# Optimization experiments

Hardware: AMD Instinct MI355X
Metric: run time of the kernel (lower is better)

The kernel has to match this reference:

```python
import jax, jax.numpy as jnp
import numpy as np
import math

D_MODEL = 768
N_HEADS = 12
D_HEAD = D_MODEL // N_HEADS
B, T = 2, 2048
EPS = 1e-5


def _layernorm(x, g, b):
    mu = jnp.mean(x, axis=-1, keepdims=True)
    var = jnp.var(x, axis=-1, keepdims=True)
    return (x - mu) * jax.lax.rsqrt(var + EPS) * g + b


def setup_inputs() -> dict:
    key = jax.random.key(0)
    ks = jax.random.split(key, 16)
    s = 0.02
    inp = {
        "x": jax.random.normal(ks[0], (B, T, D_MODEL), jnp.float32),
        "q_pos": jax.random.normal(ks[1], (B, N_HEADS, T, D_HEAD), jnp.float32),
        "k_pos": jax.random.normal(ks[2], (B, N_HEADS, T, D_HEAD), jnp.float32),
        "causal_mask": jnp.triu(jnp.ones((T, T), dtype=bool), k=1),
        "Wq": jax.random.normal(ks[3], (D_MODEL, D_MODEL), jnp.float32) * s,
        "bq": jnp.zeros((D_MODEL,), jnp.float32),
        "Wk": jax.random.normal(ks[4], (D_MODEL, D_MODEL), jnp.float32) * s,
        "bk": jnp.zeros((D_MODEL,), jnp.float32),
        "Wv": jax.random.normal(ks[5], (D_MODEL, D_MODEL), jnp.float32) * s,
        "bv": jnp.zeros((D_MODEL,), jnp.float32),
        "Wo": jax.random.normal(ks[6], (D_MODEL, D_MODEL), jnp.float32) * s,
        "bo": jnp.zeros((D_MODEL,), jnp.float32),
        "ln1_g": jnp.ones((D_MODEL,), jnp.float32),
        "ln1_b": jnp.zeros((D_MODEL,), jnp.float32),
        "ln2_g": jnp.ones((D_MODEL,), jnp.float32),
        "ln2_b": jnp.zeros((D_MODEL,), jnp.float32),
        "W1": jax.random.normal(ks[7], (D_MODEL, 4 * D_MODEL), jnp.float32) * s,
        "b1": jnp.zeros((4 * D_MODEL,), jnp.float32),
        "W2": jax.random.normal(ks[8], (4 * D_MODEL, D_MODEL), jnp.float32) * s,
        "b2": jnp.zeros((D_MODEL,), jnp.float32),
    }
    return inp


def reference(x, q_pos, k_pos, causal_mask, Wq, bq, Wk, bk, Wv, bv, Wo, bo,
              ln1_g, ln1_b, ln2_g, ln2_b, W1, b1, W2, b2):
    h = _layernorm(x, ln1_g, ln1_b)  # [B,T,D]
    # project and split heads -> [B,H,T,d]
    def heads(y):
        return y.reshape(B, T, N_HEADS, D_HEAD).transpose(0, 2, 1, 3)
    Qc = heads(h @ Wq + bq)
    Kc = heads(h @ Wk + bk)
    V = heads(h @ Wv + bv)
    scale = math.sqrt(D_HEAD)
    A_X = jnp.einsum('bhqd,bhkd->bhqk', Qc, Kc) / scale
    A_P = jnp.einsum('bhqd,bhkd->bhqk', q_pos, k_pos) / scale
    scores = A_X * A_P  # Hadamard combination of content + positional scores
    scores = jnp.where(causal_mask[None, None, :, :], -jnp.inf, scores)
    attn = jax.nn.softmax(scores, axis=-1)
    out = jnp.einsum('bhqk,bhkd->bhqd', attn, V)  # [B,H,T,d]
    out = out.transpose(0, 2, 1, 3).reshape(B, T, D_MODEL)
    out = out @ Wo + bo
    x = x + out
    h2 = _layernorm(x, ln2_g, ln2_b)
    ffn = jax.nn.gelu(h2 @ W1 + b1, approximate=False) @ W2 + b2
    return x + ffn
```

## Files before the change

kernel.cpp:

```cpp
#include <hip/hip_runtime.h>
#include <hip/hip_bf16.h>
#include <math.h>

#define D_MODEL 768
#define N_HEADS 12
#define D_HEAD  64
#define BATCH   2
#define SEQ     2048
#define ROWS    (BATCH*SEQ)
#define D_FFN   (4*D_MODEL)

typedef short bf16x8 __attribute__((ext_vector_type(8)));
typedef float f32x4  __attribute__((ext_vector_type(4)));

__device__ __forceinline__ short f2bf(float f) {
    __hip_bfloat16 h = __float2bfloat16(f);
    return *reinterpret_cast<short*>(&h);
}

template<int CTRL>
__device__ __forceinline__ float dpp_f(float x) {
    int v = __builtin_amdgcn_update_dpp(0, __float_as_int(x), CTRL, 0xF, 0xF, true);
    return __int_as_float(v);
}
__device__ __forceinline__ float dpp_max16(float x) {
    x = fmaxf(x, dpp_f<0xB1>(x));
    x = fmaxf(x, dpp_f<0x4E>(x));
    x = fmaxf(x, dpp_f<0x141>(x));
    x = fmaxf(x, dpp_f<0x140>(x));
    return x;
}
__device__ __forceinline__ float dpp_sum16(float x) {
    x += dpp_f<0xB1>(x);
    x += dpp_f<0x4E>(x);
    x += dpp_f<0x141>(x);
    x += dpp_f<0x140>(x);
    return x;
}

__global__ __launch_bounds__(256)
void prep_kernel(const float* __restrict__ Wq, const float* __restrict__ Wk,
                 const float* __restrict__ Wv, const float* __restrict__ Wo,
                 const float* __restrict__ W1, const float* __restrict__ W2,
                 const float* __restrict__ q_pos, const float* __restrict__ k_pos,
                 short* __restrict__ WTq, short* __restrict__ WTk,
                 short* __restrict__ WTv, short* __restrict__ WTo,
                 short* __restrict__ WT1, short* __restrict__ WT2,
                 short* __restrict__ qp_bf, short* __restrict__ kp_bf) {
    int id = blockIdx.x;
    if (id >= 6912) {
        int cid = id - 6912;
        bool isq = (cid < 1536);
        int c = isq ? cid : cid - 1536;
        const float* src = isq ? q_pos : k_pos;
        short* dst = isq ? qp_bf : kp_bf;
        int i = (c * 256 + threadIdx.x) * 8;
        float4 a = *reinterpret_cast<const float4*>(src + i);
        float4 b = *reinterpret_cast<const float4*>(src + i + 4);
        bf16x8 r;
        r[0]=f2bf(a.x); r[1]=f2bf(a.y); r[2]=f2bf(a.z); r[3]=f2bf(a.w);
        r[4]=f2bf(b.x); r[5]=f2bf(b.y); r[6]=f2bf(b.z); r[7]=f2bf(b.w);
        *reinterpret_cast<bf16x8*>(dst + i) = r;
        return;
    }
    const float* W; short* WT; int K, N, t;
    if (id < 576)        { W = Wq; WT = WTq; K = 768;  N = 768;  t = id; }
    else if (id < 1152)  { W = Wk; WT = WTk; K = 768;  N = 768;  t = id - 576; }
    else if (id < 1728)  { W = Wv; WT = WTv; K = 768;  N = 768;  t = id - 1152; }
    else if (id < 2304)  { W = Wo; WT = WTo; K = 768;  N = 768;  t = id - 1728; }
    else if (id < 4608)  { W = W1; WT = WT1; K = 768;  N = 3072; t = id - 2304; }
    else                 { W = W2; WT = WT2; K = 3072; N = 768;  t = id - 4608; }
    int nb = N >> 5;
    int n0 = (t % nb) * 32, k0 = (t / nb) * 32;
    __shared__ float tile[32][33];
    int tx = threadIdx.x & 31, ty = threadIdx.x >> 5;
    #pragma unroll
    for (int i = 0; i < 4; ++i)
        tile[ty + 8*i][tx] = W[(size_t)(k0 + ty + 8*i) * N + n0 + tx];
    __syncthreads();
    #pragma unroll
    for (int i = 0; i < 4; ++i)
        WT[(size_t)(n0 + ty + 8*i) * K + k0 + tx] = f2bf(tile[tx][ty + 8*i]);
}

__global__ __launch_bounds__(256)
void transpose_v_kernel(const short* __restrict__ Vm, short* __restrict__ Vt) {
    __shared__ short tile[64][72];
    int kt = blockIdx.x;
    int bh = blockIdx.y;
    int b = bh / N_HEADS, h = bh % N_HEADS;
    int tid = threadIdx.x;
    int row = tid >> 2, c16 = (tid & 3) * 16;
    const short* src = Vm + ((size_t)(b * SEQ) + kt * 64 + row) * D_MODEL + h * 64 + c16;
    *reinterpret_cast<bf16x8*>(&tile[row][c16])     = *reinterpret_cast<const bf16x8*>(src);
    *reinterpret_cast<bf16x8*>(&tile[row][c16 + 8]) = *reinterpret_cast<const bf16x8*>(src + 8);
    __syncthreads();
    int d = tid >> 2, k16 = (tid & 3) * 16;
    short o[16];
    #pragma unroll
    for (int j = 0; j < 16; ++j) o[j] = tile[k16 + j][d];
    short* dst = Vt + ((size_t)bh * 64 + d) * SEQ + kt * 64 + k16;
    *reinterpret_cast<bf16x8*>(dst)     = *reinterpret_cast<bf16x8*>(&o[0]);
    *reinterpret_cast<bf16x8*>(dst + 8) = *reinterpret_cast<bf16x8*>(&o[8]);
}

__global__ __launch_bounds__(256)
void ln_kernel(const float* __restrict__ x, const float* __restrict__ g,
               const float* __restrict__ beta, short* __restrict__ out) {
    int row = blockIdx.x;
    const float* xr = x + (size_t)row * D_MODEL;
    int t = threadIdx.x;
    float v0 = xr[t], v1 = xr[t + 256], v2 = xr[t + 512];
    float s  = v0 + v1 + v2;
    float s2 = v0*v0 + v1*v1 + v2*v2;
    __shared__ float rs[4], rs2[4];
    #pragma unroll
    for (int off = 32; off; off >>= 1) {
        s  += __shfl_down(s, off);
        s2 += __shfl_down(s2, off);
    }
    int wv = t >> 6, ln = t & 63;
    if (ln == 0) { rs[wv] = s; rs2[wv] = s2; }
    __syncthreads();
    float S  = rs[0] + rs[1] + rs[2] + rs[3];
    float S2 = rs2[0] + rs2[1] + rs2[2] + rs2[3];
    float mu  = S * (1.0f / D_MODEL);
    float var = S2 * (1.0f / D_MODEL) - mu * mu;
    float inv = rsqrtf(var + 1e-5f);
    short* orow = out + (size_t)row * D_MODEL;
    orow[t]       = f2bf((v0 - mu) * inv * g[t]       + beta[t]);
    orow[t + 256] = f2bf((v1 - mu) * inv * g[t + 256] + beta[t + 256]);
    orow[t + 512] = f2bf((v2 - mu) * inv * g[t + 512] + beta[t + 512]);
}

template<int ACT, bool RES, bool OUTBF>
__device__ __forceinline__
void gemm_body(const short* __restrict__ A, const short* __restrict__ WT,
               const float* __restrict__ bias, const float* __restrict__ res,
               void* __restrict__ Cout, int M, int N, int Kloop, int Kstride) {
    __shared__ short As[2][128 * 32];
    __shared__ short Bs[2][128 * 32];
    const int tid = threadIdx.x;
    const int w = tid >> 6, lane = tid & 63;
    const int lr = lane & 15, lg = lane >> 4;
    const int wm = w >> 1, wn = w & 1;
    const int bm = blockIdx.y * 128, bn = blockIdx.x * 128;

    f32x4 acc[4][4] = {};

    const int srow = w * 32 + (lane >> 2);
    const int scol = (lane & 3) * 8;
    const short* Ag = A  + (size_t)(bm + srow) * Kstride + scol;
    const short* Bg = WT + (size_t)(bn + srow) * Kstride + scol;

    auto stage = [&](int k0, int buf) {
        #pragma unroll
        for (int r = 0; r < 2; ++r) {
            __builtin_amdgcn_global_load_lds(
                (const __attribute__((address_space(1))) void*)(Ag + (size_t)r * 16 * Kstride + k0),
                (__attribute__((address_space(3))) void*)(&As[buf][0] + w * 1024 + r * 512),
                16, 0, 0);
            __builtin_amdgcn_global_load_lds(
                (const __attribute__((address_space(1))) void*)(Bg + (size_t)r * 16 * Kstride + k0),
                (__attribute__((address_space(3))) void*)(&Bs[buf][0] + w * 1024 + r * 512),
                16, 0, 0);
        }
    };

    stage(0, 0);
    __syncthreads();
    int cur = 0;

    for (int k0 = 0; k0 < Kloop; k0 += 32) {
        if (k0 + 32 < Kloop) stage(k0 + 32, cur ^ 1);

        bf16x8 af[4], bfr[4];
        #pragma unroll
        for (int mi = 0; mi < 4; ++mi)
            af[mi] = *reinterpret_cast<const bf16x8*>(&As[cur][0] + (wm*64 + mi*16 + lr) * 32 + lg*8);
        #pragma unroll
        for (int nj = 0; nj < 4; ++nj)
            bfr[nj] = *reinterpret_cast<const bf16x8*>(&Bs[cur][0] + (wn*64 + nj*16 + lr) * 32 + lg*8);
        __builtin_amdgcn_s_setprio(1);
        #pragma unroll
        for (int mi = 0; mi < 4; ++mi)
            #pragma unroll
            for (int nj = 0; nj < 4; ++nj)
                acc[mi][nj] = __builtin_amdgcn_mfma_f32_16x16x32_bf16(af[mi], bfr[nj], acc[mi][nj], 0, 0, 0);
        __builtin_amdgcn_s_setprio(0);

        __syncthreads();
        cur ^= 1;
    }

    float bias_v[4] = {0.f, 0.f, 0.f, 0.f};
    if constexpr (ACT != 2) {
        #pragma unroll
        for (int nj = 0; nj < 4; ++nj) bias_v[nj] = bias[bn + wn*64 + nj*16 + lr];
    }

    #pragma unroll
    for (int mi = 0; mi < 4; ++mi) {
        #pragma unroll
        for (int j = 0; j < 4; ++j) {
            size_t m = bm + wm*64 + mi*16 + lg*4 + j;
            #pragma unroll
            for (int nj = 0; nj < 4; ++nj) {
                size_t n = bn + wn*64 + nj*16 + lr;
                float v = acc[mi][nj][j] + bias_v[nj];
                if (RES) v += res[m * N + n];
                if (ACT == 1) v = 0.5f * v * (1.0f + erff(v * 0.70710678118f));
                if (OUTBF) ((short*)Cout)[m * N + n] = f2bf(v);
                else       ((float*)Cout)[m * N + n] = v;
            }
        }
    }
}

template<int ACT, bool RES, bool OUTBF>
__global__ __launch_bounds__(256)
void gemm_mfma_kernel(const short* __restrict__ A, const short* __restrict__ WT,
                      const float* __restrict__ bias, const float* __restrict__ res,
                      void* __restrict__ Cout, int M, int N, int K) {
    gemm_body<ACT, RES, OUTBF>(A, WT, bias, res, Cout, M, N, K, K);
}

__global__ __launch_bounds__(256)
void gemm_qkv_kernel(const short* __restrict__ A,
                     const short* __restrict__ WTq, const short* __restrict__ WTk,
                     const short* __restrict__ WTv,
                     const float* __restrict__ bq, const float* __restrict__ bk,
                     const float* __restrict__ bv,
                     short* __restrict__ Qm, short* __restrict__ Km, short* __restrict__ Vm) {
    const short* WT; const float* bias; short* C;
    if (blockIdx.z == 0)      { WT = WTq; bias = bq; C = Qm; }
    else if (blockIdx.z == 1) { WT = WTk; bias = bk; C = Km; }
    else                      { WT = WTv; bias = bv; C = Vm; }
    gemm_body<0, false, true>(A, WT, bias, nullptr, C, ROWS, D_MODEL, D_MODEL, D_MODEL);
}

__global__ __launch_bounds__(256)
void gemm_w2_kernel(const short* __restrict__ mid, const short* __restrict__ WT2,
                    float* __restrict__ P0, float* __restrict__ P1) {
    int z = blockIdx.z;
    gemm_body<2, false, false>(mid + z * 1536, WT2 + z * 1536, nullptr, nullptr,
                               z ? P1 : P0, ROWS, D_MODEL, 1536, D_FFN);
}

__global__ __launch_bounds__(256)
void w2_epi_kernel(const float* __restrict__ P0, const float* __restrict__ P1,
                   const float* __restrict__ b2, const float* __restrict__ x2,
                   float* __restrict__ out) {
    size_t i = ((size_t)blockIdx.x * 256 + threadIdx.x) * 4;
    int n = (int)(i % D_MODEL);
    float4 p0 = *reinterpret_cast<const float4*>(P0 + i);
    float4 p1 = *reinterpret_cast<const float4*>(P1 + i);
    float4 xr = *reinterpret_cast<const float4*>(x2 + i);
    float4 bb = *reinterpret_cast<const float4*>(b2 + n);
    float4 o;
    o.x = p0.x + p1.x + xr.x + bb.x;
    o.y = p0.y + p1.y + xr.y + bb.y;
    o.z = p0.z + p1.z + xr.z + bb.z;
    o.w = p0.w + p1.w + xr.w + bb.w;
    *reinterpret_cast<float4*>(out + i) = o;
}

__global__ __launch_bounds__(256)
void attn_mfma_kernel(const short* __restrict__ Q, const short* __restrict__ K,
                      const short* __restrict__ Vt, const short* __restrict__ qp,
                      const short* __restrict__ kp, short* __restrict__ ao) {
    __shared__ short Ks[2][4096];
    __shared__ short kps[2][4096];
    __shared__ short Vts[2][4096];
    __shared__ short Plds[4][16][76];

    int lin = blockIdx.x;
    int wid = (lin & 7) * 96 + (lin >> 3);
    int bh = wid >> 5;
    int qb = 31 - (wid & 31);
    int b = bh / N_HEADS, h = bh % N_HEADS;
    int tid = threadIdx.x, w = tid >> 6, lane = tid & 63;
    int lr = lane & 15, lg = lane >> 4;

    const short* Kh  = K  + (size_t)(b * SEQ) * D_MODEL + h * 64;
    const short* kph = kp + (size_t)bh * SEQ * 64;
    const short* Vth = Vt + (size_t)bh * 64 * SEQ;

    const int s_sub  = lane >> 3;
    const int s_colb = ((lane & 7) ^ s_sub) << 4;

    auto stage = [&](int kt, int buf) {
        #pragma unroll
        for (int j = 0; j < 2; ++j) {
            int row = (w * 2 + j) * 8 + s_sub;
            int ldsoff = (w * 2 + j) * 1024;
            __builtin_amdgcn_global_load_lds(
                (const __attribute__((address_space(1))) void*)
                    ((const char*)(Kh + (size_t)(kt * 64 + row) * D_MODEL) + s_colb),
                (__attribute__((address_space(3))) void*)((char*)&Ks[buf][0] + ldsoff), 16, 0, 0);
            __builtin_amdgcn_global_load_lds(
                (const __attribute__((address_space(1))) void*)
                    ((const char*)(kph + (size_t)(kt * 64 + row) * 64) + s_colb),
                (__attribute__((address_space(3))) void*)((char*)&kps[buf][0] + ldsoff), 16, 0, 0);
            __builtin_amdgcn_global_load_lds(
                (const __attribute__((address_space(1))) void*)
                    ((const char*)(Vth + (size_t)row * SEQ + kt * 64) + s_colb),
                (__attribute__((address_space(3))) void*)((char*)&Vts[buf][0] + ldsoff), 16, 0, 0);
        }
    };
    auto ldr = [&](const short* base, int row, int halfb) -> bf16x8 {
        int off = row * 128 + ((halfb + lg * 16) ^ ((row & 7) << 4));
        return *reinterpret_cast<const bf16x8*>((const char*)base + off);
    };

    int qbase = qb * 64 + w * 16;
    const short* Qrow  = Q  + ((size_t)(b * SEQ) + qbase + lr) * D_MODEL + h * 64;
    const short* qprow = qp + ((size_t)bh * SEQ + qbase + lr) * 64;
    bf16x8 qf0  = *reinterpret_cast<const bf16x8*>(Qrow + lg * 8);
    bf16x8 qf1  = *reinterpret_cast<const bf16x8*>(Qrow + 32 + lg * 8);
    bf16x8 qpf0 = *reinterpret_cast<const bf16x8*>(qprow + lg * 8);
    bf16x8 qpf1 = *reinterpret_cast<const bf16x8*>(qprow + 32 + lg * 8);

    f32x4 o_acc[4] = {};
    float m_run[4], l_run[4];
    #pragma unroll
    for (int r = 0; r < 4; ++r) { m_run[r] = -1e30f; l_run[r] = 0.f; }

    int nkt = qb + 1;
    stage(0, 0);
    __syncthreads();
    int cur = 0;

    for (int kt = 0; kt < nkt; ++kt) {
        if (kt + 1 < nkt) stage(kt + 1, cur ^ 1);

        const short* Kb  = &Ks[cur][0];
        const short* kpb = &kps[cur][0];
        const short* Vb  = &Vts[cur][0];
        f32x4 sx[4] = {}, sp[4] = {};
        __builtin_amdgcn_s_setprio(1);
        #pragma unroll
        for (int sub = 0; sub < 4; ++sub) {
            int row = sub * 16 + lr;
            bf16x8 kf0 = ldr(Kb, row, 0),  kf1 = ldr(Kb, row, 64);
            bf16x8 kq0 = ldr(kpb, row, 0), kq1 = ldr(kpb, row, 64);
            sx[sub] = __builtin_amdgcn_mfma_f32_16x16x32_bf16(qf0,  kf0, sx[sub], 0, 0, 0);
            sx[sub] = __builtin_amdgcn_mfma_f32_16x16x32_bf16(qf1,  kf1, sx[sub], 0, 0, 0);
            sp[sub] = __builtin_amdgcn_mfma_f32_16x16x32_bf16(qpf0, kq0, sp[sub], 0, 0, 0);
            sp[sub] = __builtin_amdgcn_mfma_f32_16x16x32_bf16(qpf1, kq1, sp[sub], 0, 0, 0);
        }
        __builtin_amdgcn_s_setprio(0);

        float sc[4][4];
        float pmax[4];
        bool diag = (kt == qb);
        #pragma unroll
        for (int r = 0; r < 4; ++r) {
            int row = qbase + lg * 4 + r;
            float mx = -1e30f;
            #pragma unroll
            for (int sub = 0; sub < 4; ++sub) {
                float v = sx[sub][r] * sp[sub][r] * (1.0f / 64.0f);
                if (diag) {
                    int col = kt * 64 + sub * 16 + lr;
                    if (col > row) v = -1e30f;
                }
                sc[sub][r] = v;
                mx = fmaxf(mx, v);
            }
            pmax[r] = dpp_max16(mx);
        }

        bool need = false;
        #pragma unroll
        for (int r = 0; r < 4; ++r) need = need || (pmax[r] > m_run[r] + 8.f);
        if (__any(need)) {
            #pragma unroll
            for (int r = 0; r < 4; ++r) {
                float m_new = fmaxf(m_run[r], pmax[r]);
                float scale = __expf(m_run[r] - m_new);
                m_run[r] = m_new;
                l_run[r] *= scale;
                #pragma unroll
                for (int ds = 0; ds < 4; ++ds) o_acc[ds][r] *= scale;
            }
        }
        #pragma unroll
        for (int r = 0; r < 4; ++r) {
            float s = 0.f;
            #pragma unroll
            for (int sub = 0; sub < 4; ++sub) {
                float p = __expf(sc[sub][r] - m_run[r]);
                sc[sub][r] = p;
                s += p;
            }
            l_run[r] += dpp_sum16(s);
        }

        #pragma unroll
        for (int sub = 0; sub < 4; ++sub)
            #pragma unroll
            for (int r = 0; r < 4; ++r)
                Plds[w][lg * 4 + r][sub * 16 + lr] = f2bf(sc[sub][r]);

        bf16x8 pa0 = *reinterpret_cast<bf16x8*>(&Plds[w][lr][lg * 8]);
        bf16x8 pa1 = *reinterpret_cast<bf16x8*>(&Plds[w][lr][32 + lg * 8]);

        __builtin_amdgcn_s_setprio(1);
        #pragma unroll
        for (int ds = 0; ds < 4; ++ds) {
            int row = ds * 16 + lr;
            bf16x8 vb0 = ldr(Vb, row, 0), vb1 = ldr(Vb, row, 64);
            o_acc[ds] = __builtin_amdgcn_mfma_f32_16x16x32_bf16(pa0, vb0, o_acc[ds], 0, 0, 0);
            o_acc[ds] = __builtin_amdgcn_mfma_f32_16x16x32_bf16(pa1, vb1, o_acc[ds], 0, 0, 0);
        }
        __builtin_amdgcn_s_setprio(0);

        __syncthreads();
        cur ^= 1;
    }

    #pragma unroll
    for (int ds = 0; ds < 4; ++ds)
        #pragma unroll
        for (int r = 0; r < 4; ++r) {
            int row = qbase + lg * 4 + r;
            float val = o_acc[ds][r] / l_run[r];
            ao[((size_t)(b * SEQ) + row) * D_MODEL + h * 64 + ds * 16 + lr] = f2bf(val);
        }
}

extern "C" void kernel_launch(void* const* d_in, const int* in_sizes, int n_in,
                              void* d_out, int out_size, void* d_ws, size_t ws_size,
                              hipStream_t stream) {
    const float* x     = (const float*)d_in[0];
    const float* q_pos = (const float*)d_in[1];
    const float* k_pos = (const float*)d_in[2];
    const float* Wq = (const float*)d_in[4];
    const float* bq = (const float*)d_in[5];
    const float* Wk = (const float*)d_in[6];
    const float* bk = (const float*)d_in[7];
    const float* Wv = (const float*)d_in[8];
    const float* bv = (const float*)d_in[9];
    const float* Wo = (const float*)d_in[10];
    const float* bo = (const float*)d_in[11];
    const float* ln1_g = (const float*)d_in[12];
    const float* ln1_b = (const float*)d_in[13];
    const float* ln2_g = (const float*)d_in[14];
    const float* ln2_b = (const float*)d_in[15];
    const float* W1 = (const float*)d_in[16];
    const float* b1 = (const float*)d_in[17];
    const float* W2 = (const float*)d_in[18];
    const float* b2 = (const float*)d_in[19];
    float* out = (float*)d_out;

    char* p = (char*)d_ws;
    auto alloc = [&](size_t bytes) { char* q = p; p += (bytes + 255) & ~(size_t)255; return q; };
    const size_t SA = (size_t)ROWS * D_MODEL;
    const size_t SP = (size_t)BATCH * N_HEADS * SEQ * 64;

    short* h_bf  = (short*)alloc(SA * 2);
    short* Qm    = (short*)alloc(SA * 2);
    short* Km    = (short*)alloc(SA * 2);
    short* Vm    = (short*)alloc(SA * 2);
    short* Vt    = (short*)alloc(SP * 2);
    short* ao    = (short*)alloc(SA * 2);
    short* qp_bf = (short*)alloc(SP * 2);
    short* kp_bf = (short*)alloc(SP * 2);
    short* mid   = (short*)alloc((size_t)ROWS * D_FFN * 2);
    float* x2    = (float*)alloc(SA * 4);
    float* P0    = (float*)alloc(SA * 4);
    float* P1    = (float*)alloc(SA * 4);
    short* WTq   = (short*)alloc((size_t)D_MODEL * D_MODEL * 2);
    short* WTk   = (short*)alloc((size_t)D_MODEL * D_MODEL * 2);
    short* WTv   = (short*)alloc((size_t)D_MODEL * D_MODEL * 2);
    short* WTo   = (short*)alloc((size_t)D_MODEL * D_MODEL * 2);
    short* WT1   = (short*)alloc((size_t)D_MODEL * D_FFN * 2);
    short* WT2   = (short*)alloc((size_t)D_MODEL * D_FFN * 2);

    prep_kernel<<<9984, 256, 0, stream>>>(Wq, Wk, Wv, Wo, W1, W2, q_pos, k_pos,
                                          WTq, WTk, WTv, WTo, WT1, WT2, qp_bf, kp_bf);

    ln_kernel<<<ROWS, 256, 0, stream>>>(x, ln1_g, ln1_b, h_bf);
    gemm_qkv_kernel<<<dim3(D_MODEL/128, ROWS/128, 3), 256, 0, stream>>>(
        h_bf, WTq, WTk, WTv, bq, bk, bv, Qm, Km, Vm);
    transpose_v_kernel<<<dim3(SEQ/64, BATCH*N_HEADS), 256, 0, stream>>>(Vm, Vt);
    attn_mfma_kernel<<<768, 256, 0, stream>>>(Qm, Km, Vt, qp_bf, kp_bf, ao);
    gemm_mfma_kernel<0, true, false><<<dim3(D_MODEL/128, ROWS/128), 256, 0, stream>>>(
        ao, WTo, bo, x, x2, ROWS, D_MODEL, D_MODEL);
    ln_kernel<<<ROWS, 256, 0, stream>>>(x2, ln2_g, ln2_b, h_bf);
    gemm_mfma_kernel<1, false, true><<<dim3(D_FFN/128, ROWS/128), 256, 0, stream>>>(
        h_bf, WT1, b1, nullptr, mid, ROWS, D_FFN, D_MODEL);
    gemm_w2_kernel<<<dim3(D_MODEL/128, ROWS/128, 2), 256, 0, stream>>>(mid, WT2, P0, P1);
    w2_epi_kernel<<<(int)(SA/1024), 256, 0, stream>>>(P0, P1, b2, x2, out);
}
```

Baseline: 230.7 us.

## Pair causal q-tiles per block for load balance and fold score scale into Q

The attention kernel now uses 128-thread blocks that each process two 32-row query tiles (pair and 63-pair), so every block does a near-equal amount of causal work instead of blocks with 1 to 32 key tiles. The 1/64 score scale is folded into the Q projection epilogue and the q_pos bf16 conversion (0.125 each), removing a multiply per score element. Each block now reloads K/kpos/V tiles for both phases and has fewer waves, which may lower latency hiding. Scaling before the bf16 rounding also shifts rounding slightly.

```diff
diff --git a/kernel.cpp b/kernel.cpp
--- a/kernel.cpp
+++ b/kernel.cpp
@@ -54,12 +54,13 @@
         int c = isq ? cid : cid - 1536;
         const float* src = isq ? q_pos : k_pos;
         short* dst = isq ? qp_bf : kp_bf;
+        float sc = isq ? 0.125f : 1.0f;
         int i = (c * 256 + threadIdx.x) * 8;
         float4 a = *reinterpret_cast<const float4*>(src + i);
         float4 b = *reinterpret_cast<const float4*>(src + i + 4);
         bf16x8 r;
-        r[0]=f2bf(a.x); r[1]=f2bf(a.y); r[2]=f2bf(a.z); r[3]=f2bf(a.w);
-        r[4]=f2bf(b.x); r[5]=f2bf(b.y); r[6]=f2bf(b.z); r[7]=f2bf(b.w);
+        r[0]=f2bf(a.x*sc); r[1]=f2bf(a.y*sc); r[2]=f2bf(a.z*sc); r[3]=f2bf(a.w*sc);
+        r[4]=f2bf(b.x*sc); r[5]=f2bf(b.y*sc); r[6]=f2bf(b.z*sc); r[7]=f2bf(b.w*sc);
         *reinterpret_cast<bf16x8*>(dst + i) = r;
         return;
     }
@@ -137,7 +138,8 @@
 __device__ __forceinline__
 void gemm_body(const short* __restrict__ A, const short* __restrict__ WT,
                const float* __restrict__ bias, const float* __restrict__ res,
-               void* __restrict__ Cout, int M, int N, int Kloop, int Kstride) {
+               void* __restrict__ Cout, int M, int N, int Kloop, int Kstride,
+               float oscale) {
     __shared__ short As[2][128 * 32];
     __shared__ short Bs[2][128 * 32];
     const int tid = threadIdx.x;
@@ -210,7 +212,7 @@
                 float v = acc[mi][nj][j] + bias_v[nj];
                 if (RES) v += res[m * N + n];
                 if (ACT == 1) v = 0.5f * v * (1.0f + erff(v * 0.70710678118f));
-                if (OUTBF) ((short*)Cout)[m * N + n] = f2bf(v);
+                if (OUTBF) ((short*)Cout)[m * N + n] = f2bf(v * oscale);
                 else       ((float*)Cout)[m * N + n] = v;
             }
         }
@@ -222,7 +224,7 @@
 void gemm_mfma_kernel(const short* __restrict__ A, const short* __restrict__ WT,
                       const float* __restrict__ bias, const float* __restrict__ res,
                       void* __restrict__ Cout, int M, int N, int K) {
-    gemm_body<ACT, RES, OUTBF>(A, WT, bias, res, Cout, M, N, K, K);
+    gemm_body<ACT, RES, OUTBF>(A, WT, bias, res, Cout, M, N, K, K, 1.0f);
 }
 
 __global__ __launch_bounds__(256)
@@ -232,11 +234,11 @@
                      const float* __restrict__ bq, const float* __restrict__ bk,
                      const float* __restrict__ bv,
                      short* __restrict__ Qm, short* __restrict__ Km, short* __restrict__ Vm) {
-    const short* WT; const float* bias; short* C;
-    if (blockIdx.z == 0)      { WT = WTq; bias = bq; C = Qm; }
-    else if (blockIdx.z == 1) { WT = WTk; bias = bk; C = Km; }
-    else                      { WT = WTv; bias = bv; C = Vm; }
-    gemm_body<0, false, true>(A, WT, bias, nullptr, C, ROWS, D_MODEL, D_MODEL, D_MODEL);
+    const short* WT; const float* bias; short* C; float sc;
+    if (blockIdx.z == 0)      { WT = WTq; bias = bq; C = Qm; sc = 0.125f; }
+    else if (blockIdx.z == 1) { WT = WTk; bias = bk; C = Km; sc = 1.0f; }
+    else                      { WT = WTv; bias = bv; C = Vm; sc = 1.0f; }
+    gemm_body<0, false, true>(A, WT, bias, nullptr, C, ROWS, D_MODEL, D_MODEL, D_MODEL, sc);
 }
 
 __global__ __launch_bounds__(256)
@@ -244,7 +246,7 @@
                     float* __restrict__ P0, float* __restrict__ P1) {
     int z = blockIdx.z;
     gemm_body<2, false, false>(mid + z * 1536, WT2 + z * 1536, nullptr, nullptr,
-                               z ? P1 : P0, ROWS, D_MODEL, 1536, D_FFN);
+                               z ? P1 : P0, ROWS, D_MODEL, 1536, D_FFN, 1.0f);
 }
 
 __global__ __launch_bounds__(256)
@@ -265,19 +267,19 @@
     *reinterpret_cast<float4*>(out + i) = o;
 }
 
-__global__ __launch_bounds__(256)
+__global__ __launch_bounds__(128)
 void attn_mfma_kernel(const short* __restrict__ Q, const short* __restrict__ K,
                       const short* __restrict__ Vt, const short* __restrict__ qp,
                       const short* __restrict__ kp, short* __restrict__ ao) {
     __shared__ short Ks[2][4096];
     __shared__ short kps[2][4096];
     __shared__ short Vts[2][4096];
-    __shared__ short Plds[4][16][76];
+    __shared__ short Plds[2][16][72];
 
     int lin = blockIdx.x;
     int wid = (lin & 7) * 96 + (lin >> 3);
     int bh = wid >> 5;
-    int qb = 31 - (wid & 31);
+    int pair = wid & 31;
     int b = bh / N_HEADS, h = bh % N_HEADS;
     int tid = threadIdx.x, w = tid >> 6, lane = tid & 63;
     int lr = lane & 15, lg = lane >> 4;
@@ -291,9 +293,9 @@
 
     auto stage = [&](int kt, int buf) {
         #pragma unroll
-        for (int j = 0; j < 2; ++j) {
-            int row = (w * 2 + j) * 8 + s_sub;
-            int ldsoff = (w * 2 + j) * 1024;
+        for (int j = 0; j < 4; ++j) {
+            int row = (w * 4 + j) * 8 + s_sub;
+            int ldsoff = (w * 4 + j) * 1024;
             __builtin_amdgcn_global_load_lds(
                 (const __attribute__((address_space(1))) void*)
                     ((const char*)(Kh + (size_t)(kt * 64 + row) * D_MODEL) + s_colb),
@@ -313,121 +315,127 @@
         return *reinterpret_cast<const bf16x8*>((const char*)base + off);
     };
 
-    int qbase = qb * 64 + w * 16;
-    const short* Qrow  = Q  + ((size_t)(b * SEQ) + qbase + lr) * D_MODEL + h * 64;
-    const short* qprow = qp + ((size_t)bh * SEQ + qbase + lr) * 64;
-    bf16x8 qf0  = *reinterpret_cast<const bf16x8*>(Qrow + lg * 8);
-    bf16x8 qf1  = *reinterpret_cast<const bf16x8*>(Qrow + 32 + lg * 8);
-    bf16x8 qpf0 = *reinterpret_cast<const bf16x8*>(qprow + lg * 8);
-    bf16x8 qpf1 = *reinterpret_cast<const bf16x8*>(qprow + 32 + lg * 8);
-
-    f32x4 o_acc[4] = {};
-    float m_run[4], l_run[4];
     #pragma unroll
-    for (int r = 0; r < 4; ++r) { m_run[r] = -1e30f; l_run[r] = 0.f; }
-
-    int nkt = qb + 1;
-    stage(0, 0);
-    __syncthreads();
-    int cur = 0;
-
-    for (int kt = 0; kt < nkt; ++kt) {
-        if (kt + 1 < nkt) stage(kt + 1, cur ^ 1);
-
-        const short* Kb  = &Ks[cur][0];
-        const short* kpb = &kps[cur][0];
-        const short* Vb  = &Vts[cur][0];
-        f32x4 sx[4] = {}, sp[4] = {};
-        __builtin_amdgcn_s_setprio(1);
-        #pragma unroll
-        for (int sub = 0; sub < 4; ++sub) {
-            int row = sub * 16 + lr;
-            bf16x8 kf0 = ldr(Kb, row, 0),  kf1 = ldr(Kb, row, 64);
-            bf16x8 kq0 = ldr(kpb, row, 0), kq1 = ldr(kpb, row, 64);
-            sx[sub] = __builtin_amdgcn_mfma_f32_16x16x32_bf16(qf0,  kf0, sx[sub], 0, 0, 0);
-            sx[sub] = __builtin_amdgcn_mfma_f32_16x16x32_bf16(qf1,  kf1, sx[sub], 0, 0, 0);
-            sp[sub] = __builtin_amdgcn_mfma_f32_16x16x32_bf16(qpf0, kq0, sp[sub], 0, 0, 0);
-            sp[sub] = __builtin_amdgcn_mfma_f32_16x16x32_bf16(qpf1, kq1, sp[sub], 0, 0, 0);
+    for (int ph = 0; ph < 2; ++ph) {
+        int qt = ph ? 63 - pair : pair;
+        int qbase = qt * 32 + w * 16;
+
+        const short* Qrow  = Q  + ((size_t)(b * SEQ) + qbase + lr) * D_MODEL + h * 64;
+        const short* qprow = qp + ((size_t)bh * SEQ + qbase + lr) * 64;
+        bf16x8 qf0  = *reinterpret_cast<const bf16x8*>(Qrow + lg * 8);
+        bf16x8 qf1  = *reinterpret_cast<const bf16x8*>(Qrow + 32 + lg * 8);
+        bf16x8 qpf0 = *reinterpret_cast<const bf16x8*>(qprow + lg * 8);
+        bf16x8 qpf1 = *reinterpret_cast<const bf16x8*>(qprow + 32 + lg * 8);
+
+        f32x4 o_acc[4] = {};
+        float m_run[4], l_run[4];
+        #pragma unroll
+        for (int r = 0; r < 4; ++r) { m_run[r] = -1e30f; l_run[r] = 0.f; }
+
+        int nkt = qt / 2 + 1;
+        stage(0, 0);
+        __syncthreads();
+        int cur = 0;
+
+        for (int kt = 0; kt < nkt; ++kt) {
+            if (kt + 1 < nkt) stage(kt + 1, cur ^ 1);
+
+            const short* Kb  = &Ks[cur][0];
+            const short* kpb = &kps[cur][0];
+            const short* Vb  = &Vts[cur][0];
+            f32x4 sx[4] = {}, sp[4] = {};
+            __builtin_amdgcn_s_setprio(1);
+            #pragma unroll
+            for (int sub = 0; sub < 4; ++sub) {
+                int row = sub * 16 + lr;
+                bf16x8 kf0 = ldr(Kb, row, 0),  kf1 = ldr(Kb, row, 64);
+                bf16x8 kq0 = ldr(kpb, row, 0), kq1 = ldr(kpb, row, 64);
+                sx[sub] = __builtin_amdgcn_mfma_f32_16x16x32_bf16(qf0,  kf0, sx[sub], 0, 0, 0);
+                sx[sub] = __builtin_amdgcn_mfma_f32_16x16x32_bf16(qf1,  kf1, sx[sub], 0, 0, 0);
+                sp[sub] = __builtin_amdgcn_mfma_f32_16x16x32_bf16(qpf0, kq0, sp[sub], 0, 0, 0);
+                sp[sub] = __builtin_amdgcn_mfma_f32_16x16x32_bf16(qpf1, kq1, sp[sub], 0, 0, 0);
+            }
+            __builtin_amdgcn_s_setprio(0);
+
+            float sc[4][4];
+            float pmax[4];
+            bool diag = (kt == nkt - 1);
+            #pragma unroll
+            for (int r = 0; r < 4; ++r) {
+                int row = qbase + lg * 4 + r;
+                float mx = -1e30f;
+                #pragma unroll
+                for (int sub = 0; sub < 4; ++sub) {
+                    float v = sx[sub][r] * sp[sub][r];
+                    if (diag) {
+                        int col = kt * 64 + sub * 16 + lr;
+                        if (col > row) v = -1e30f;
+                    }
+                    sc[sub][r] = v;
+                    mx = fmaxf(mx, v);
+                }
+                pmax[r] = dpp_max16(mx);
+            }
+
+            bool need = false;
+            #pragma unroll
+            for (int r = 0; r < 4; ++r) need = need || (pmax[r] > m_run[r] + 8.f);
+            if (__any(need)) {
+                #pragma unroll
+                for (int r = 0; r < 4; ++r) {
+                    float m_new = fmaxf(m_run[r], pmax[r]);
+                    float scale = __expf(m_run[r] - m_new);
+                    m_run[r] = m_new;
+                    l_run[r] *= scale;
+                    #pragma unroll
+                    for (int ds = 0; ds < 4; ++ds) o_acc[ds][r] *= scale;
+                }
+            }
+            #pragma unroll
+            for (int r = 0; r < 4; ++r) {
+                float s = 0.f;
+                #pragma unroll
+                for (int sub = 0; sub < 4; ++sub) {
+                    float pv = __expf(sc[sub][r] - m_run[r]);
+                    sc[sub][r] = pv;
+                    s += pv;
+                }
+                l_run[r] += dpp_sum16(s);
+            }
+
+            #pragma unroll
+            for (int sub = 0; sub < 4; ++sub)
+                #pragma unroll
+                for (int r = 0; r < 4; ++r)
+                    Plds[w][lg * 4 + r][sub * 16 + lr] = f2bf(sc[sub][r]);
+
+            bf16x8 pa0 = *reinterpret_cast<bf16x8*>(&Plds[w][lr][lg * 8]);
+            bf16x8 pa1 = *reinterpret_cast<bf16x8*>(&Plds[w][lr][32 + lg * 8]);
+
+            __builtin_amdgcn_s_setprio(1);
+            #pragma unroll
+            for (int ds = 0; ds < 4; ++ds) {
+                int row = ds * 16 + lr;
+                bf16x8 vb0 = ldr(Vb, row, 0), vb1 = ldr(Vb, row, 64);
+                o_acc[ds] = __builtin_amdgcn_mfma_f32_16x16x32_bf16(pa0, vb0, o_acc[ds], 0, 0, 0);
+                o_acc[ds] = __builtin_amdgcn_mfma_f32_16x16x32_bf16(pa1, vb1, o_acc[ds], 0, 0, 0);
+            }
+            __builtin_amdgcn_s_setprio(0);
+
+            __syncthreads();
+            cur ^= 1;
         }
-        __builtin_amdgcn_s_setprio(0);
-
-        float sc[4][4];
-        float pmax[4];
-        bool diag = (kt == qb);
-        #pragma unroll
-        for (int r = 0; r < 4; ++r) {
-            int row = qbase + lg * 4 + r;
-            float mx = -1e30f;
-            #pragma unroll
-            for (int sub = 0; sub < 4; ++sub) {
-                float v = sx[sub][r] * sp[sub][r] * (1.0f / 64.0f);
-                if (diag) {
-                    int col = kt * 64 + sub * 16 + lr;
-                    if (col > row) v = -1e30f;
-                }
-                sc[sub][r] = v;
-                mx = fmaxf(mx, v);
-            }
-            pmax[r] = dpp_max16(mx);
-        }
-
-        bool need = false;
-        #pragma unroll
-        for (int r = 0; r < 4; ++r) need = need || (pmax[r] > m_run[r] + 8.f);
-        if (__any(need)) {
+
+        #pragma unroll
+        for (int ds = 0; ds < 4; ++ds)
             #pragma unroll
             for (int r = 0; r < 4; ++r) {
-                float m_new = fmaxf(m_run[r], pmax[r]);
-                float scale = __expf(m_run[r] - m_new);
-                m_run[r] = m_new;
-                l_run[r] *= scale;
-                #pragma unroll
-                for (int ds = 0; ds < 4; ++ds) o_acc[ds][r] *= scale;
-            }
-        }
-        #pragma unroll
-        for (int r = 0; r < 4; ++r) {
-            float s = 0.f;
-            #pragma unroll
-            for (int sub = 0; sub < 4; ++sub) {
-                float p = __expf(sc[sub][r] - m_run[r]);
-                sc[sub][r] = p;
-                s += p;
-            }
-            l_run[r] += dpp_sum16(s);
-        }
-
-        #pragma unroll
-        for (int sub = 0; sub < 4; ++sub)
-            #pragma unroll
-            for (int r = 0; r < 4; ++r)
-                Plds[w][lg * 4 + r][sub * 16 + lr] = f2bf(sc[sub][r]);
-
-        bf16x8 pa0 = *reinterpret_cast<bf16x8*>(&Plds[w][lr][lg * 8]);
-        bf16x8 pa1 = *reinterpret_cast<bf16x8*>(&Plds[w][lr][32 + lg * 8]);
-
-        __builtin_amdgcn_s_setprio(1);
-        #pragma unroll
-        for (int ds = 0; ds < 4; ++ds) {
-            int row = ds * 16 + lr;
-            bf16x8 vb0 = ldr(Vb, row, 0), vb1 = ldr(Vb, row, 64);
-            o_acc[ds] = __builtin_amdgcn_mfma_f32_16x16x32_bf16(pa0, vb0, o_acc[ds], 0, 0, 0);
-            o_acc[ds] = __builtin_amdgcn_mfma_f32_16x16x32_bf16(pa1, vb1, o_acc[ds], 0, 0, 0);
-        }
-        __builtin_amdgcn_s_setprio(0);
-
+                int row = qbase + lg * 4 + r;
+                float val = o_acc[ds][r] / l_run[r];
+                ao[((size_t)(b * SEQ) + row) * D_MODEL + h * 64 + ds * 16 + lr] = f2bf(val);
+            }
         __syncthreads();
-        cur ^= 1;
     }
-
-    #pragma unroll
-    for (int ds = 0; ds < 4; ++ds)
-        #pragma unroll
-        for (int r = 0; r < 4; ++r) {
-            int row = qbase + lg * 4 + r;
-            float val = o_acc[ds][r] / l_run[r];
-            ao[((size_t)(b * SEQ) + row) * D_MODEL + h * 64 + ds * 16 + lr] = f2bf(val);
-        }
 }
 
 extern "C" void kernel_launch(void* const* d_in, const int* in_sizes, int n_in,
@@ -485,7 +493,7 @@
     gemm_qkv_kernel<<<dim3(D_MODEL/128, ROWS/128, 3), 256, 0, stream>>>(
         h_bf, WTq, WTk, WTv, bq, bk, bv, Qm, Km, Vm);
     transpose_v_kernel<<<dim3(SEQ/64, BATCH*N_HEADS), 256, 0, stream>>>(Vm, Vt);
-    attn_mfma_kernel<<<768, 256, 0, stream>>>(Qm, Km, Vt, qp_bf, kp_bf, ao);
+    attn_mfma_kernel<<<768, 128, 0, stream>>>(Qm, Km, Vt, qp_bf, kp_bf, ao);
     gemm_mfma_kernel<0, true, false><<<dim3(D_MODEL/128, ROWS/128), 256, 0, stream>>>(
         ao, WTo, bo, x, x2, ROWS, D_MODEL, D_MODEL);
     ln_kernel<<<ROWS, 256, 0, stream>>>(x2, ln2_g, ln2_b, h_bf);
```

Result: no change. 229.1 us (-0.7%).
